# Optimization experiments

Measured on AMD Instinct MI355X. Metric: run time of the kernel, lower is better.

Reference implementation:

```python
import jax, jax.numpy as jnp
import numpy as np


def setup_inputs() -> dict:
    key = jax.random.key(0)
    k1, k2, k3, k4, k5 = jax.random.split(key, 5)
    B, L, G, DG = 2, 8192, 256, 8
    D = G * DG
    x1 = jax.random.normal(k1, (B, L, G, DG), dtype=jnp.float32)
    x2 = jax.random.normal(k2, (B, L, G, DG), dtype=jnp.float32)
    v = jax.random.normal(k3, (B, L, G, DG), dtype=jnp.float32)
    # implicit/explicit filter output: one length-L kernel per group, scaled down
    # like a decaying long-conv filter so outputs stay O(1)
    t = jnp.arange(L, dtype=jnp.float32)
    decay = jnp.exp(-t / 1024.0)[None, :]  # (1, L)
    h = jax.random.normal(k4, (G, L), dtype=jnp.float32) * decay / jnp.sqrt(jnp.float32(L))
    conv_bias = jax.random.normal(k5, (D,), dtype=jnp.float32)
    return {"x1": x1, "x2": x2, "v": v, "h": h, "conv_bias": conv_bias}


def reference(x1, x2, v, h, conv_bias):
    # x1, x2, v: (B, L, G, DG); h: (G, L); conv_bias: (G*DG,)
    B, L, G, DG = x1.shape
    D = G * DG
    # 'b l g dg -> b (g dg) l'
    x1c = x1.reshape(B, L, D).transpose(0, 2, 1)  # (B, D, L)
    x2c = x2.reshape(B, L, D).transpose(0, 2, 1)
    vc = v.reshape(B, L, D).transpose(0, 2, 1)

    kv = x2c * vc  # pre-gate: (B, D, L)

    fft_size = 2 * L  # causal (linear) convolution via zero-padded FFT
    # each group's filter is shared across its DG channels
    h_rep = jnp.repeat(h, DG, axis=0)  # (D, L)
    kv_f = jnp.fft.rfft(kv.astype(jnp.float32), n=fft_size)
    h_f = jnp.fft.rfft(h_rep.astype(jnp.float32), n=fft_size)
    y = jnp.fft.irfft(kv_f * h_f[None], n=fft_size)[..., :L]  # (B, D, L)

    y = y + kv * conv_bias[None, :, None]  # skip/bias term
    z = x1c * y  # post-gate (identity gating activation)

    # back to (B, L, D)
    return z.transpose(0, 2, 1)
```

## Files before the change

kernel.cpp:

```cpp
#include <hip/hip_runtime.h>
#include <hip/hip_bf16.h>

typedef __attribute__((ext_vector_type(8))) __bf16 bf16x8;
typedef __attribute__((ext_vector_type(4))) __bf16 bf16x4;
typedef __attribute__((ext_vector_type(4))) float  f32x4;

#define L_LEN   8192
#define D_DIM   2048
#define G_NUM   256
#define HP      8320
#define HS      808
#define KVS     264

__global__ __launch_bounds__(256) void prep_kv_kernel(
    const float* __restrict__ x2, const float* __restrict__ v,
    __bf16* __restrict__ kvout)
{
  const int tid = threadIdx.x;
  const int l0 = blockIdx.x << 6;
  const int d0 = blockIdx.y << 6;
  const int b  = blockIdx.z;
  const int dl = tid & 63;
  const int lc = tid >> 6;
  const int gch = d0 + dl;
  const int row = ((gch >> 3) << 4) + (b << 3) + (gch & 7);
  const size_t ibase = ((size_t)(b * L_LEN + l0 + (lc << 4))) * D_DIM + gch;
  bf16x8 a0, a1;
#pragma unroll
  for (int k = 0; k < 8; ++k) {
    const size_t i0 = ibase + (size_t)k * D_DIM;
    const size_t i1 = ibase + (size_t)(k + 8) * D_DIM;
    a0[k] = (__bf16)(x2[i0] * v[i0]);
    a1[k] = (__bf16)(x2[i1] * v[i1]);
  }
  __bf16* dst = kvout + (size_t)row * L_LEN + l0 + (lc << 4);
  *(bf16x8*)dst = a0;
  *(bf16x8*)(dst + 8) = a1;
}

__global__ __launch_bounds__(256) void prep_h_kernel(
    const float* __restrict__ h, __bf16* __restrict__ hr)
{
  const unsigned i = blockIdx.x * 256u + threadIdx.x;
  const unsigned g = i / (8u * HP);
  const unsigned r = i - g * (8u * HP);
  const unsigned s = r / HP;
  const unsigned z = r - s * HP;
  const int P = 8255 - (int)z - (int)s;
  __bf16 val = (__bf16)0.0f;
  if (P >= 0 && P < 8192) val = (__bf16)h[(size_t)g * 8192 + P];
  hr[i] = val;
}

__global__ __launch_bounds__(256, 4) void conv_kernel(
    const __bf16* __restrict__ KV, const __bf16* __restrict__ HR,
    const float* __restrict__ x1, const float* __restrict__ bias,
    float* __restrict__ out)
{
  __shared__ __bf16 sKV[16 * KVS];
  __shared__ __bf16 sH[8 * HS];

  const int g   = blockIdx.x;
  const int jb  = 15 - (int)blockIdx.y;
  const int l0  = jb << 9;
  const int tid = threadIdx.x;
  const int lane = tid & 63, wv = tid >> 6;
  const int m = lane & 15, q = lane >> 4;

  const __bf16* __restrict__ KVg = KV + (size_t)g * (16 * L_LEN);
  const __bf16* __restrict__ HRg = HR + (size_t)g * (8 * HP);

  f32x4 acc0 = {0.f,0.f,0.f,0.f}, acc1 = acc0, acc2 = acc0, acc3 = acc0,
        acc4 = acc0, acc5 = acc0, acc6 = acc0, acc7 = acc0;

  bf16x8 zed;
#pragma unroll
  for (int k = 0; k < 8; ++k) zed[k] = (__bf16)0.0f;

  const int cst = tid >> 4, tst = (tid & 15) << 3;
  const int s_c   = (7 - m) & 7;
  const int bbase = m * KVS + (q << 3);
  const int wend  = l0 + (wv << 7) + 128;

  const int send = l0 + 512;
  for (int tb = 0; tb < send; tb += 256) {
    __syncthreads();
    {
      const __bf16* src = &KVg[cst * L_LEN + tb + tst];
      *(bf16x8*)&sKV[cst * KVS + tst]       = *(const bf16x8*)src;
      *(bf16x8*)&sKV[cst * KVS + tst + 128] = *(const bf16x8*)(src + 128);
    }
    const int Bv = 8255 - l0 + tb;
    const int Y0 = (Bv - 518) & ~7;
    for (int u = tid; u < 8 * 98; u += 256) {
      const int s   = u / 98;
      const int off = (u - s * 98) << 3;
      const int yy  = Y0 + off;
      bf16x8 w = zed;
      if (yy + 8 <= HP) w = *(const bf16x8*)&HRg[s * HP + yy];
      *(bf16x8*)&sH[s * HS + off] = w;
    }
    __syncthreads();

    if (tb >= wend) continue;

    const int zbase = Bv - (wv << 7) - m + (q << 3);
    const int abase = s_c * HS + (zbase - s_c - Y0) - 112;

#define AFR(f) (*(const bf16x8*)&sH[abase + ((f) << 4)])
#define BFR(j) (*(const bf16x8*)&sKV[bbase + ((j) << 5)])
#define MF(ac, ar) ac = __builtin_amdgcn_mfma_f32_16x16x32_bf16(ar, bq, ac, 0, 0, 0)
    bf16x8 a0=AFR(0),a1=AFR(1),a2=AFR(2),a3=AFR(3),a4=AFR(4),a5=AFR(5),a6=AFR(6),a7=AFR(7);
    bf16x8 bq;
    bq = BFR(0);
    MF(acc0,a7); MF(acc1,a6); MF(acc2,a5); MF(acc3,a4); MF(acc4,a3); MF(acc5,a2); MF(acc6,a1); MF(acc7,a0);
    a0 = AFR(8);  a1 = AFR(9);  bq = BFR(1);
    MF(acc0,a1); MF(acc1,a0); MF(acc2,a7); MF(acc3,a6); MF(acc4,a5); MF(acc5,a4); MF(acc6,a3); MF(acc7,a2);
    a2 = AFR(10); a3 = AFR(11); bq = BFR(2);
    MF(acc0,a3); MF(acc1,a2); MF(acc2,a1); MF(acc3,a0); MF(acc4,a7); MF(acc5,a6); MF(acc6,a5); MF(acc7,a4);
    a4 = AFR(12); a5 = AFR(13); bq = BFR(3);
    MF(acc0,a5); MF(acc1,a4); MF(acc2,a3); MF(acc3,a2); MF(acc4,a1); MF(acc5,a0); MF(acc6,a7); MF(acc7,a6);
    a6 = AFR(14); a7 = AFR(15); bq = BFR(4);
    MF(acc0,a7); MF(acc1,a6); MF(acc2,a5); MF(acc3,a4); MF(acc4,a3); MF(acc5,a2); MF(acc6,a1); MF(acc7,a0);
    a0 = AFR(16); a1 = AFR(17); bq = BFR(5);
    MF(acc0,a1); MF(acc1,a0); MF(acc2,a7); MF(acc3,a6); MF(acc4,a5); MF(acc5,a4); MF(acc6,a3); MF(acc7,a2);
    a2 = AFR(18); a3 = AFR(19); bq = BFR(6);
    MF(acc0,a3); MF(acc1,a2); MF(acc2,a1); MF(acc3,a0); MF(acc4,a7); MF(acc5,a6); MF(acc6,a5); MF(acc7,a4);
    a4 = AFR(20); a5 = AFR(21); bq = BFR(7);
    MF(acc0,a5); MF(acc1,a4); MF(acc2,a3); MF(acc3,a2); MF(acc4,a1); MF(acc5,a0); MF(acc6,a7); MF(acc7,a6);
#undef MF
#undef BFR
#undef AFR
  }

  const int c = m;
  const int bb = c >> 3, dg = c & 7;
  const float bv = bias[(g << 3) + dg];

#define CONV_EPI(i, accv) {                                                     \
    const int l = l0 + (wv << 7) + ((i) << 4) + (q << 2);                       \
    const bf16x4 kv4 = *(const bf16x4*)&KVg[c * L_LEN + l];                     \
    for (int r = 0; r < 4; ++r) {                                               \
      const float y = accv[r] + (float)kv4[r] * bv;                             \
      const size_t oidx = ((size_t)(bb * L_LEN + l + r)) * D_DIM + (g << 3) + dg;\
      out[oidx] = x1[oidx] * y;                                                 \
    } }

  CONV_EPI(0, acc0)
  CONV_EPI(1, acc1)
  CONV_EPI(2, acc2)
  CONV_EPI(3, acc3)
  CONV_EPI(4, acc4)
  CONV_EPI(5, acc5)
  CONV_EPI(6, acc6)
  CONV_EPI(7, acc7)
#undef CONV_EPI
}

extern "C" void kernel_launch(void* const* d_in, const int* in_sizes, int n_in,
                              void* d_out, int out_size, void* d_ws, size_t ws_size,
                              hipStream_t stream)
{
  const float* x1 = (const float*)d_in[0];
  const float* x2 = (const float*)d_in[1];
  const float* v  = (const float*)d_in[2];
  const float* h  = (const float*)d_in[3];
  const float* cb = (const float*)d_in[4];
  float* out = (float*)d_out;

  __bf16* kv = (__bf16*)d_ws;
  __bf16* hr = kv + (size_t)G_NUM * 16 * L_LEN;

  prep_kv_kernel<<<dim3(L_LEN / 64, D_DIM / 64, 2), 256, 0, stream>>>(x2, v, kv);
  prep_h_kernel<<<(G_NUM * 8 * HP) / 256, 256, 0, stream>>>(h, hr);
  conv_kernel<<<dim3(G_NUM, 16), 256, 0, stream>>>(kv, hr, x1, cb, out);
}
```

Measured before the change: 720.8 us.

## Double-buffer conv LDS tiles with register prefetch; transpose kv prep through LDS

The conv kernel now uses two LDS buffers and prefetches the next KV and filter tiles into registers while the MFMA loop runs on the current tile. This overlaps global loads with compute and cuts the barriers per step from two to one. The prep_kv kernel now reads x2 and v with vectorized float4 row loads and transposes through a swizzled LDS tile, replacing strided scalar loads. The costs are doubled shared memory, more registers and a lower occupancy hint (3 blocks per SIMD group instead of 4).

Measured after the change: 694.3 us. -3.7%, faster.

```diff
diff --git a/kernel.cpp b/kernel.cpp
--- a/kernel.cpp
+++ b/kernel.cpp
@@ -16,26 +16,46 @@
     const float* __restrict__ x2, const float* __restrict__ v,
     __bf16* __restrict__ kvout)
 {
+  __shared__ __bf16 sT[128 * 64];
   const int tid = threadIdx.x;
-  const int l0 = blockIdx.x << 6;
+  const int l0 = blockIdx.x << 7;
   const int d0 = blockIdx.y << 6;
   const int b  = blockIdx.z;
-  const int dl = tid & 63;
-  const int lc = tid >> 6;
-  const int gch = d0 + dl;
-  const int row = ((gch >> 3) << 4) + (b << 3) + (gch & 7);
-  const size_t ibase = ((size_t)(b * L_LEN + l0 + (lc << 4))) * D_DIM + gch;
-  bf16x8 a0, a1;
-#pragma unroll
-  for (int k = 0; k < 8; ++k) {
-    const size_t i0 = ibase + (size_t)k * D_DIM;
-    const size_t i1 = ibase + (size_t)(k + 8) * D_DIM;
-    a0[k] = (__bf16)(x2[i0] * v[i0]);
-    a1[k] = (__bf16)(x2[i1] * v[i1]);
+  const int lr = tid >> 4;
+  const int dq = tid & 15;
+#pragma unroll
+  for (int p = 0; p < 8; ++p) {
+    const int ll = (p << 4) + lr;
+    const size_t idx = ((size_t)(b * L_LEN + l0 + ll)) * D_DIM + d0 + (dq << 2);
+    const f32x4 a = *(const f32x4*)&x2[idx];
+    const f32x4 c = *(const f32x4*)&v[idx];
+    bf16x4 kvv;
+    kvv[0] = (__bf16)(a[0] * c[0]);
+    kvv[1] = (__bf16)(a[1] * c[1]);
+    kvv[2] = (__bf16)(a[2] * c[2]);
+    kvv[3] = (__bf16)(a[3] * c[3]);
+    *(bf16x4*)&sT[(ll << 6) + (((dq ^ (ll >> 3)) & 15) << 2)] = kvv;
   }
-  __bf16* dst = kvout + (size_t)row * L_LEN + l0 + (lc << 4);
-  *(bf16x8*)dst = a0;
-  *(bf16x8*)(dst + 8) = a1;
+  __syncthreads();
+#pragma unroll
+  for (int p = 0; p < 2; ++p) {
+    const int c  = tid + (p << 8);
+    const int r  = c >> 3, seg = c & 7;
+    const int rb = r >> 2, rl = r & 3;
+    const int gch = d0 + r;
+    const int row = ((gch >> 3) << 4) + (b << 3) + (gch & 7);
+    bf16x8 w0, w1;
+#pragma unroll
+    for (int j = 0; j < 8; ++j) {
+      const int lj0 = (seg << 4) + j;
+      const int lj1 = lj0 + 8;
+      w0[j] = sT[(lj0 << 6) + (((rb ^ (lj0 >> 3)) & 15) << 2) + rl];
+      w1[j] = sT[(lj1 << 6) + (((rb ^ (lj1 >> 3)) & 15) << 2) + rl];
+    }
+    __bf16* dst = kvout + (size_t)row * L_LEN + l0 + (seg << 4);
+    *(bf16x8*)dst = w0;
+    *(bf16x8*)(dst + 8) = w1;
+  }
 }
 
 __global__ __launch_bounds__(256) void prep_h_kernel(
@@ -52,13 +72,13 @@
   hr[i] = val;
 }
 
-__global__ __launch_bounds__(256, 4) void conv_kernel(
+__global__ __launch_bounds__(256, 3) void conv_kernel(
     const __bf16* __restrict__ KV, const __bf16* __restrict__ HR,
     const float* __restrict__ x1, const float* __restrict__ bias,
     float* __restrict__ out)
 {
-  __shared__ __bf16 sKV[16 * KVS];
-  __shared__ __bf16 sH[8 * HS];
+  __shared__ __bf16 sKV[2][16 * KVS];
+  __shared__ __bf16 sH[2][8 * HS];
 
   const int g   = blockIdx.x;
   const int jb  = 15 - (int)blockIdx.y;
@@ -82,56 +102,89 @@
   const int bbase = m * KVS + (q << 3);
   const int wend  = l0 + (wv << 7) + 128;
 
-  const int send = l0 + 512;
-  for (int tb = 0; tb < send; tb += 256) {
-    __syncthreads();
-    {
-      const __bf16* src = &KVg[cst * L_LEN + tb + tst];
-      *(bf16x8*)&sKV[cst * KVS + tst]       = *(const bf16x8*)src;
-      *(bf16x8*)&sKV[cst * KVS + tst + 128] = *(const bf16x8*)(src + 128);
-    }
-    const int Bv = 8255 - l0 + tb;
-    const int Y0 = (Bv - 518) & ~7;
-    for (int u = tid; u < 8 * 98; u += 256) {
-      const int s   = u / 98;
-      const int off = (u - s * 98) << 3;
-      const int yy  = Y0 + off;
-      bf16x8 w = zed;
-      if (yy + 8 <= HP) w = *(const bf16x8*)&HRg[s * HP + yy];
-      *(bf16x8*)&sH[s * HS + off] = w;
-    }
-    __syncthreads();
-
-    if (tb >= wend) continue;
-
-    const int zbase = Bv - (wv << 7) - m + (q << 3);
-    const int abase = s_c * HS + (zbase - s_c - Y0) - 112;
-
-#define AFR(f) (*(const bf16x8*)&sH[abase + ((f) << 4)])
-#define BFR(j) (*(const bf16x8*)&sKV[bbase + ((j) << 5)])
+  const int u0 = tid, u1 = tid + 256, u2 = tid + 512, u3 = tid + 768;
+  const int sh0 = u0 / 98, sh1 = u1 / 98, sh2 = u2 / 98, sh3 = u3 / 98;
+  const int o0 = (u0 - sh0 * 98) << 3, o1 = (u1 - sh1 * 98) << 3;
+  const int o2 = (u2 - sh2 * 98) << 3, o3 = (u3 - sh3 * 98) << 3;
+  const int w0 = sh0 * HS + o0, w1 = sh1 * HS + o1;
+  const int w2 = sh2 * HS + o2, w3 = sh3 * HS + o3;
+  const bool vld3 = (u3 < 8 * 98);
+
+  const int nt = (l0 + 512) >> 8;
+
+  bf16x8 pkv0, pkv1, ph0, ph1, ph2, ph3;
+
+#define STAGE_LOAD(tbn) do {                                                     \
+    const int Bvn = 8255 - l0 + (tbn);                                           \
+    const int Y0n = (Bvn - 518) & ~7;                                            \
+    pkv0 = *(const bf16x8*)&KVg[cst * L_LEN + (tbn) + tst];                      \
+    pkv1 = *(const bf16x8*)&KVg[cst * L_LEN + (tbn) + tst + 128];                \
+    int yy;                                                                      \
+    yy = Y0n + o0; ph0 = (yy + 8 <= HP) ? *(const bf16x8*)&HRg[sh0 * HP + yy] : zed; \
+    yy = Y0n + o1; ph1 = (yy + 8 <= HP) ? *(const bf16x8*)&HRg[sh1 * HP + yy] : zed; \
+    yy = Y0n + o2; ph2 = (yy + 8 <= HP) ? *(const bf16x8*)&HRg[sh2 * HP + yy] : zed; \
+    yy = Y0n + o3; ph3 = (vld3 && yy + 8 <= HP) ? *(const bf16x8*)&HRg[sh3 * HP + yy] : zed; \
+  } while (0)
+
+#define STAGE_WRITE(bi) do {                                                     \
+    *(bf16x8*)&sKV[bi][cst * KVS + tst]       = pkv0;                            \
+    *(bf16x8*)&sKV[bi][cst * KVS + tst + 128] = pkv1;                            \
+    *(bf16x8*)&sH[bi][w0] = ph0;                                                 \
+    *(bf16x8*)&sH[bi][w1] = ph1;                                                 \
+    *(bf16x8*)&sH[bi][w2] = ph2;                                                 \
+    if (vld3) *(bf16x8*)&sH[bi][w3] = ph3;                                       \
+  } while (0)
+
+  STAGE_LOAD(0);
+  STAGE_WRITE(0);
+  __syncthreads();
+
+  int cur = 0;
+  for (int t = 0; t < nt; ++t) {
+    const int tb = t << 8;
+    const bool pf = (t + 1 < nt);
+    if (pf) STAGE_LOAD(tb + 256);
+
+    if (tb < wend) {
+      const __bf16* __restrict__ sHc  = sH[cur];
+      const __bf16* __restrict__ sKVc = sKV[cur];
+      const int Bv = 8255 - l0 + tb;
+      const int Y0 = (Bv - 518) & ~7;
+      const int zbase = Bv - (wv << 7) - m + (q << 3);
+      const int abase = s_c * HS + (zbase - s_c - Y0) - 112;
+
+#define AFR(f) (*(const bf16x8*)&sHc[abase + ((f) << 4)])
+#define BFR(j) (*(const bf16x8*)&sKVc[bbase + ((j) << 5)])
 #define MF(ac, ar) ac = __builtin_amdgcn_mfma_f32_16x16x32_bf16(ar, bq, ac, 0, 0, 0)
-    bf16x8 a0=AFR(0),a1=AFR(1),a2=AFR(2),a3=AFR(3),a4=AFR(4),a5=AFR(5),a6=AFR(6),a7=AFR(7);
-    bf16x8 bq;
-    bq = BFR(0);
-    MF(acc0,a7); MF(acc1,a6); MF(acc2,a5); MF(acc3,a4); MF(acc4,a3); MF(acc5,a2); MF(acc6,a1); MF(acc7,a0);
-    a0 = AFR(8);  a1 = AFR(9);  bq = BFR(1);
-    MF(acc0,a1); MF(acc1,a0); MF(acc2,a7); MF(acc3,a6); MF(acc4,a5); MF(acc5,a4); MF(acc6,a3); MF(acc7,a2);
-    a2 = AFR(10); a3 = AFR(11); bq = BFR(2);
-    MF(acc0,a3); MF(acc1,a2); MF(acc2,a1); MF(acc3,a0); MF(acc4,a7); MF(acc5,a6); MF(acc6,a5); MF(acc7,a4);
-    a4 = AFR(12); a5 = AFR(13); bq = BFR(3);
-    MF(acc0,a5); MF(acc1,a4); MF(acc2,a3); MF(acc3,a2); MF(acc4,a1); MF(acc5,a0); MF(acc6,a7); MF(acc7,a6);
-    a6 = AFR(14); a7 = AFR(15); bq = BFR(4);
-    MF(acc0,a7); MF(acc1,a6); MF(acc2,a5); MF(acc3,a4); MF(acc4,a3); MF(acc5,a2); MF(acc6,a1); MF(acc7,a0);
-    a0 = AFR(16); a1 = AFR(17); bq = BFR(5);
-    MF(acc0,a1); MF(acc1,a0); MF(acc2,a7); MF(acc3,a6); MF(acc4,a5); MF(acc5,a4); MF(acc6,a3); MF(acc7,a2);
-    a2 = AFR(18); a3 = AFR(19); bq = BFR(6);
-    MF(acc0,a3); MF(acc1,a2); MF(acc2,a1); MF(acc3,a0); MF(acc4,a7); MF(acc5,a6); MF(acc6,a5); MF(acc7,a4);
-    a4 = AFR(20); a5 = AFR(21); bq = BFR(7);
-    MF(acc0,a5); MF(acc1,a4); MF(acc2,a3); MF(acc3,a2); MF(acc4,a1); MF(acc5,a0); MF(acc6,a7); MF(acc7,a6);
+      bf16x8 a0=AFR(0),a1=AFR(1),a2=AFR(2),a3=AFR(3),a4=AFR(4),a5=AFR(5),a6=AFR(6),a7=AFR(7);
+      bf16x8 bq;
+      bq = BFR(0);
+      MF(acc0,a7); MF(acc1,a6); MF(acc2,a5); MF(acc3,a4); MF(acc4,a3); MF(acc5,a2); MF(acc6,a1); MF(acc7,a0);
+      a0 = AFR(8);  a1 = AFR(9);  bq = BFR(1);
+      MF(acc0,a1); MF(acc1,a0); MF(acc2,a7); MF(acc3,a6); MF(acc4,a5); MF(acc5,a4); MF(acc6,a3); MF(acc7,a2);
+      a2 = AFR(10); a3 = AFR(11); bq = BFR(2);
+      MF(acc0,a3); MF(acc1,a2); MF(acc2,a1); MF(acc3,a0); MF(acc4,a7); MF(acc5,a6); MF(acc6,a5); MF(acc7,a4);
+      a4 = AFR(12); a5 = AFR(13); bq = BFR(3);
+      MF(acc0,a5); MF(acc1,a4); MF(acc2,a3); MF(acc3,a2); MF(acc4,a1); MF(acc5,a0); MF(acc6,a7); MF(acc7,a6);
+      a6 = AFR(14); a7 = AFR(15); bq = BFR(4);
+      MF(acc0,a7); MF(acc1,a6); MF(acc2,a5); MF(acc3,a4); MF(acc4,a3); MF(acc5,a2); MF(acc6,a1); MF(acc7,a0);
+      a0 = AFR(16); a1 = AFR(17); bq = BFR(5);
+      MF(acc0,a1); MF(acc1,a0); MF(acc2,a7); MF(acc3,a6); MF(acc4,a5); MF(acc5,a4); MF(acc6,a3); MF(acc7,a2);
+      a2 = AFR(18); a3 = AFR(19); bq = BFR(6);
+      MF(acc0,a3); MF(acc1,a2); MF(acc2,a1); MF(acc3,a0); MF(acc4,a7); MF(acc5,a6); MF(acc6,a5); MF(acc7,a4);
+      a4 = AFR(20); a5 = AFR(21); bq = BFR(7);
+      MF(acc0,a5); MF(acc1,a4); MF(acc2,a3); MF(acc3,a2); MF(acc4,a1); MF(acc5,a0); MF(acc6,a7); MF(acc7,a6);
 #undef MF
 #undef BFR
 #undef AFR
+    }
+
+    if (pf) STAGE_WRITE(cur ^ 1);
+    __syncthreads();
+    cur ^= 1;
   }
+#undef STAGE_LOAD
+#undef STAGE_WRITE
 
   const int c = m;
   const int bb = c >> 3, dg = c & 7;
@@ -171,7 +224,7 @@
   __bf16* kv = (__bf16*)d_ws;
   __bf16* hr = kv + (size_t)G_NUM * 16 * L_LEN;
 
-  prep_kv_kernel<<<dim3(L_LEN / 64, D_DIM / 64, 2), 256, 0, stream>>>(x2, v, kv);
+  prep_kv_kernel<<<dim3(L_LEN / 128, D_DIM / 64, 2), 256, 0, stream>>>(x2, v, kv);
   prep_h_kernel<<<(G_NUM * 8 * HP) / 256, 256, 0, stream>>>(h, hr);
   conv_kernel<<<dim3(G_NUM, 16), 256, 0, stream>>>(kv, hr, x1, cb, out);
 }
```
